# Performance work log

Measured on AMD Instinct MI355X. Metric: run time of the kernel, lower is better.

## Reference

```python
import jax, jax.numpy as jnp
import numpy as np

N = 1281167        # memory bank size (ImageNet train set)
NEGS = 4096        # negatives per sample
PROJ_DIM = 128
TEMPERATURE = 0.07
BATCH = 256


def setup_inputs() -> dict:
    key = jax.random.key(0)
    k1, k2, k3, k4 = jax.random.split(key, 4)
    proj = jax.random.normal(k1, (BATCH, PROJ_DIM), dtype=jnp.float32)
    proj = proj / jnp.linalg.norm(proj, axis=-1, keepdims=True)
    bank = jax.random.normal(k2, (N, PROJ_DIM), dtype=jnp.float32)
    bank = bank / jnp.linalg.norm(bank, axis=-1, keepdims=True)
    pos_index = jax.random.randint(k3, (BATCH,), 0, N)
    idx = jax.random.randint(k4, (BATCH, NEGS + 1), 0, N)
    idx = idx.at[:, 0].set(pos_index)  # first column is the positive sample
    return {"proj": proj, "bank": bank, "idx": idx}


def reference(proj, bank, idx):
    # gather (negs+1) bank rows per batch element: [B, negs+1, D]
    samples = bank[idx]
    # batched dot product: [B, negs+1]
    sim = jnp.einsum('bkd,bd->bk', samples, proj)
    out = jnp.exp(sim / TEMPERATURE)
    # z is estimated once from the first batch and treated as a constant
    z = jax.lax.stop_gradient(out.mean()) * N
    output = out / z
    m = NEGS / N  # noise prior ratio Pn(i)*negs
    p_d = jnp.log(output[:, 0] / (output[:, 0] + m))          # [B]
    p_n = jnp.log(m / (output[:, 1:] + m))                    # [B, negs]
    loss = -(p_d.sum() + p_n.sum()) / BATCH
    pos_samples = samples[:, 0]                               # [B, D]
    return loss, pos_samples
```

## Files before the change

### kernel.cpp

```cpp
#include <hip/hip_runtime.h>
#include <math.h>

#define N_BANK   1281167
#define NEGS     4096
#define K_TOT    (NEGS + 1)
#define PROJ_DIM 128
#define BATCH    256
#define CHUNKS   16
#define KCH      ((K_TOT + CHUNKS - 1) / CHUNKS)
#define GRID_MAIN (BATCH * CHUNKS)
#define NVEC     ((BATCH * K_TOT) / 4)
#define GRID_LOSS ((NVEC + 255) / 256)

#define WS_MAINPART(ws) ((double*)(ws))
#define WS_LOSSPART(ws) ((double*)((char*)(ws) + 32768))
#define WS_EXPV(ws)     ((float*)((char*)(ws) + 65536))

__device__ __forceinline__ double block_reduce_bcast(double v, double* swred, int tid)
{
    for (int off = 32; off > 0; off >>= 1) v += __shfl_down(v, off);
    if ((tid & 63) == 0) swred[tid >> 6] = v;
    __syncthreads();
    double r = swred[0] + swred[1] + swred[2] + swred[3];
    __syncthreads();
    return r;
}

__global__ __launch_bounds__(256) void npid_main(
    const float* __restrict__ proj, const float* __restrict__ bank,
    const int* __restrict__ idx, float* __restrict__ out,
    float* __restrict__ expv, double* __restrict__ mainpart)
{
    const int b     = blockIdx.x >> 4;
    const int chunk = blockIdx.x & 15;
    const int tid   = threadIdx.x;
    const int group = tid >> 4;
    const int lane  = tid & 15;

    __shared__ int    sidx[KCH];
    __shared__ double swred[4];

    const int k0     = chunk * KCH;
    const int kcount = (k0 + KCH <= K_TOT) ? KCH : (K_TOT - k0);

    for (int t = tid; t < kcount; t += 256)
        sidx[t] = idx[b * K_TOT + k0 + t];
    __syncthreads();

    const float* pr = proj + b * PROJ_DIM;
    float4 p0 = *(const float4*)(pr + 4 * lane);
    float4 p1 = *(const float4*)(pr + 64 + 4 * lane);

    double dsum = 0.0;
    int j = group;
    for (; j + 16 < kcount; j += 32) {
        const int r0 = sidx[j];
        const int r1 = sidx[j + 16];
        const float* br0 = bank + (long long)r0 * PROJ_DIM;
        const float* br1 = bank + (long long)r1 * PROJ_DIM;
        float4 a0 = *(const float4*)(br0 + 4 * lane);
        float4 a1 = *(const float4*)(br0 + 64 + 4 * lane);
        float4 c0 = *(const float4*)(br1 + 4 * lane);
        float4 c1 = *(const float4*)(br1 + 64 + 4 * lane);

        float s0 = p0.x*a0.x + p0.y*a0.y + p0.z*a0.z + p0.w*a0.w
                 + p1.x*a1.x + p1.y*a1.y + p1.z*a1.z + p1.w*a1.w;
        float s1 = p0.x*c0.x + p0.y*c0.y + p0.z*c0.z + p0.w*c0.w
                 + p1.x*c1.x + p1.y*c1.y + p1.z*c1.z + p1.w*c1.w;

        s0 += __shfl_xor(s0, 1);  s1 += __shfl_xor(s1, 1);
        s0 += __shfl_xor(s0, 2);  s1 += __shfl_xor(s1, 2);
        s0 += __shfl_xor(s0, 4);  s1 += __shfl_xor(s1, 4);
        s0 += __shfl_xor(s0, 8);  s1 += __shfl_xor(s1, 8);

        if (lane == 0) {
            float e0 = expf(s0 * (1.0f / 0.07f));
            float e1 = expf(s1 * (1.0f / 0.07f));
            expv[b * K_TOT + k0 + j]      = e0;
            expv[b * K_TOT + k0 + j + 16] = e1;
            dsum += (double)e0 + (double)e1;
        }
    }
    for (; j < kcount; j += 16) {
        const int r0 = sidx[j];
        const float* br0 = bank + (long long)r0 * PROJ_DIM;
        float4 a0 = *(const float4*)(br0 + 4 * lane);
        float4 a1 = *(const float4*)(br0 + 64 + 4 * lane);
        float s0 = p0.x*a0.x + p0.y*a0.y + p0.z*a0.z + p0.w*a0.w
                 + p1.x*a1.x + p1.y*a1.y + p1.z*a1.z + p1.w*a1.w;
        s0 += __shfl_xor(s0, 1);
        s0 += __shfl_xor(s0, 2);
        s0 += __shfl_xor(s0, 4);
        s0 += __shfl_xor(s0, 8);
        if (lane == 0) {
            float e0 = expf(s0 * (1.0f / 0.07f));
            expv[b * K_TOT + k0 + j] = e0;
            dsum += (double)e0;
        }
    }

    if (chunk == 0 && group == 0) {
        const int row = sidx[0];
        const float* br = bank + (long long)row * PROJ_DIM;
        *(float4*)(out + 1 + b * PROJ_DIM + 4 * lane)      = *(const float4*)(br + 4 * lane);
        *(float4*)(out + 1 + b * PROJ_DIM + 64 + 4 * lane) = *(const float4*)(br + 64 + 4 * lane);
    }

    double bsum = block_reduce_bcast(dsum, swred, tid);
    if (tid == 0) mainpart[blockIdx.x] = bsum;
}

__global__ __launch_bounds__(256) void npid_loss(
    const float* __restrict__ expv, const double* __restrict__ mainpart,
    double* __restrict__ losspart)
{
    const int tid = threadIdx.x;
    __shared__ double swred[4];

    double zs = 0.0;
    for (int t = tid; t < GRID_MAIN; t += 256) zs += mainpart[t];
    const double esum = block_reduce_bcast(zs, swred, tid);

    const double z  = (esum / (double)(BATCH * K_TOT)) * (double)N_BANK;
    const double mz = ((double)NEGS / (double)N_BANK) * z;
    const float inv_mz = (float)(1.0 / mz);

    const int i = blockIdx.x * 256 + tid;
    double local = 0.0;
    if (i < NVEC) {
        float4 o = ((const float4*)expv)[i];
        float t = log1pf(o.x * inv_mz) + log1pf(o.y * inv_mz)
                + log1pf(o.z * inv_mz) + log1pf(o.w * inv_mz);
        local = -(double)t;
    }

    double bsum = block_reduce_bcast(local, swred, tid);
    if (tid == 0) losspart[blockIdx.x] = bsum;
}

__global__ __launch_bounds__(256) void npid_final(
    const float* __restrict__ expv, const double* __restrict__ mainpart,
    const double* __restrict__ losspart, float* __restrict__ out)
{
    const int tid = threadIdx.x;
    __shared__ double swred[4];

    double zs = 0.0;
    for (int t = tid; t < GRID_MAIN; t += 256) zs += mainpart[t];
    const double esum = block_reduce_bcast(zs, swred, tid);

    const double z  = (esum / (double)(BATCH * K_TOT)) * (double)N_BANK;
    const double mz = ((double)NEGS / (double)N_BANK) * z;

    double lsum = 0.0;
    for (int t = tid; t < GRID_LOSS; t += 256) lsum += losspart[t];

    const double o = (double)expv[tid * K_TOT];
    lsum += log1p(o / mz) - log1p(mz / o);

    double total = block_reduce_bcast(lsum, swred, tid);
    if (tid == 0) out[0] = (float)(-total / (double)BATCH);
}

extern "C" void kernel_launch(void* const* d_in, const int* in_sizes, int n_in,
                              void* d_out, int out_size, void* d_ws, size_t ws_size,
                              hipStream_t stream)
{
    const float* proj = (const float*)d_in[0];
    const float* bank = (const float*)d_in[1];
    const int*   idx  = (const int*)d_in[2];
    float* out = (float*)d_out;

    double* mainpart = WS_MAINPART(d_ws);
    double* losspart = WS_LOSSPART(d_ws);
    float*  expv     = WS_EXPV(d_ws);

    npid_main <<<GRID_MAIN, 256, 0, stream>>>(proj, bank, idx, out, expv, mainpart);
    npid_loss <<<GRID_LOSS, 256, 0, stream>>>(expv, mainpart, losspart);
    npid_final<<<1, 256, 0, stream>>>(expv, mainpart, losspart, out);
}
```

Before: 98.20 us.

## Sweep bank gathers in three address bands for cache locality

The main kernel now makes three passes over each block's index list and only gathers rows whose bank index falls in the current third of the bank. The aim is to keep concurrent blocks working on a smaller region of the 656MB bank at once, so the gathers hit in the last-level cache more often. It also halves the chunk count per batch row, asks for 8 blocks per CU through launch bounds, drops the two-row unroll, and fuses the positive-row copy into the loop. The cost is three scans of the shared index array with divergent branches. Blocks are not synchronised with each other, so the band locality across the GPU may be weak.

```diff
diff --git a/kernel.cpp b/kernel.cpp
--- a/kernel.cpp
+++ b/kernel.cpp
@@ -6,14 +6,17 @@
 #define K_TOT    (NEGS + 1)
 #define PROJ_DIM 128
 #define BATCH    256
-#define CHUNKS   16
+#define CHUNKS   8
 #define KCH      ((K_TOT + CHUNKS - 1) / CHUNKS)
 #define GRID_MAIN (BATCH * CHUNKS)
 #define NVEC     ((BATCH * K_TOT) / 4)
 #define GRID_LOSS ((NVEC + 255) / 256)
 
+#define SPLIT1   427056
+#define SPLIT2   854112
+
 #define WS_MAINPART(ws) ((double*)(ws))
-#define WS_LOSSPART(ws) ((double*)((char*)(ws) + 32768))
+#define WS_LOSSPART(ws) ((double*)((char*)(ws) + 16384))
 #define WS_EXPV(ws)     ((float*)((char*)(ws) + 65536))
 
 __device__ __forceinline__ double block_reduce_bcast(double v, double* swred, int tid)
@@ -26,13 +29,13 @@
     return r;
 }
 
-__global__ __launch_bounds__(256) void npid_main(
+__global__ __launch_bounds__(256, 8) void npid_main(
     const float* __restrict__ proj, const float* __restrict__ bank,
     const int* __restrict__ idx, float* __restrict__ out,
     float* __restrict__ expv, double* __restrict__ mainpart)
 {
-    const int b     = blockIdx.x >> 4;
-    const int chunk = blockIdx.x & 15;
+    const int b     = blockIdx.x >> 3;
+    const int chunk = blockIdx.x & 7;
     const int tid   = threadIdx.x;
     const int group = tid >> 4;
     const int lane  = tid & 15;
@@ -52,58 +55,39 @@
     float4 p1 = *(const float4*)(pr + 64 + 4 * lane);
 
     double dsum = 0.0;
-    int j = group;
-    for (; j + 16 < kcount; j += 32) {
-        const int r0 = sidx[j];
-        const int r1 = sidx[j + 16];
-        const float* br0 = bank + (long long)r0 * PROJ_DIM;
-        const float* br1 = bank + (long long)r1 * PROJ_DIM;
-        float4 a0 = *(const float4*)(br0 + 4 * lane);
-        float4 a1 = *(const float4*)(br0 + 64 + 4 * lane);
-        float4 c0 = *(const float4*)(br1 + 4 * lane);
-        float4 c1 = *(const float4*)(br1 + 64 + 4 * lane);
 
-        float s0 = p0.x*a0.x + p0.y*a0.y + p0.z*a0.z + p0.w*a0.w
-                 + p1.x*a1.x + p1.y*a1.y + p1.z*a1.z + p1.w*a1.w;
-        float s1 = p0.x*c0.x + p0.y*c0.y + p0.z*c0.z + p0.w*c0.w
-                 + p1.x*c1.x + p1.y*c1.y + p1.z*c1.z + p1.w*c1.w;
+    #pragma unroll
+    for (int sweep = 0; sweep < 3; ++sweep) {
+        const int lo = (sweep == 0) ? 0      : (sweep == 1 ? SPLIT1 : SPLIT2);
+        const int hi = (sweep == 0) ? SPLIT1 : (sweep == 1 ? SPLIT2 : N_BANK);
 
-        s0 += __shfl_xor(s0, 1);  s1 += __shfl_xor(s1, 1);
-        s0 += __shfl_xor(s0, 2);  s1 += __shfl_xor(s1, 2);
-        s0 += __shfl_xor(s0, 4);  s1 += __shfl_xor(s1, 4);
-        s0 += __shfl_xor(s0, 8);  s1 += __shfl_xor(s1, 8);
+        for (int j = group; j < kcount; j += 16) {
+            const int row = sidx[j];
+            if (row >= lo && row < hi) {
+                const float* br = bank + (long long)row * PROJ_DIM;
+                float4 a0 = *(const float4*)(br + 4 * lane);
+                float4 a1 = *(const float4*)(br + 64 + 4 * lane);
 
-        if (lane == 0) {
-            float e0 = expf(s0 * (1.0f / 0.07f));
-            float e1 = expf(s1 * (1.0f / 0.07f));
-            expv[b * K_TOT + k0 + j]      = e0;
-            expv[b * K_TOT + k0 + j + 16] = e1;
-            dsum += (double)e0 + (double)e1;
+                float s = p0.x*a0.x + p0.y*a0.y + p0.z*a0.z + p0.w*a0.w
+                        + p1.x*a1.x + p1.y*a1.y + p1.z*a1.z + p1.w*a1.w;
+
+                s += __shfl_xor(s, 1);
+                s += __shfl_xor(s, 2);
+                s += __shfl_xor(s, 4);
+                s += __shfl_xor(s, 8);
+
+                if (lane == 0) {
+                    float e = expf(s * (1.0f / 0.07f));
+                    expv[b * K_TOT + k0 + j] = e;
+                    dsum += (double)e;
+                }
+
+                if (chunk == 0 && j == 0) {
+                    *(float4*)(out + 1 + b * PROJ_DIM + 4 * lane)      = a0;
+                    *(float4*)(out + 1 + b * PROJ_DIM + 64 + 4 * lane) = a1;
+                }
+            }
         }
-    }
-    for (; j < kcount; j += 16) {
-        const int r0 = sidx[j];
-        const float* br0 = bank + (long long)r0 * PROJ_DIM;
-        float4 a0 = *(const float4*)(br0 + 4 * lane);
-        float4 a1 = *(const float4*)(br0 + 64 + 4 * lane);
-        float s0 = p0.x*a0.x + p0.y*a0.y + p0.z*a0.z + p0.w*a0.w
-                 + p1.x*a1.x + p1.y*a1.y + p1.z*a1.z + p1.w*a1.w;
-        s0 += __shfl_xor(s0, 1);
-        s0 += __shfl_xor(s0, 2);
-        s0 += __shfl_xor(s0, 4);
-        s0 += __shfl_xor(s0, 8);
-        if (lane == 0) {
-            float e0 = expf(s0 * (1.0f / 0.07f));
-            expv[b * K_TOT + k0 + j] = e0;
-            dsum += (double)e0;
-        }
-    }
-
-    if (chunk == 0 && group == 0) {
-        const int row = sidx[0];
-        const float* br = bank + (long long)row * PROJ_DIM;
-        *(float4*)(out + 1 + b * PROJ_DIM + 4 * lane)      = *(const float4*)(br + 4 * lane);
-        *(float4*)(out + 1 + b * PROJ_DIM + 64 + 4 * lane) = *(const float4*)(br + 64 + 4 * lane);
     }
 
     double bsum = block_reduce_bcast(dsum, swred, tid);
```

Result: slower. 106.0 us (+7.9%).
